# Optimization experiments

Measured on AMD Instinct MI355X. Metric: run time of the kernel, lower is better.

Reference implementation:

```python
import jax, jax.numpy as jnp
import numpy as np

B, S, E, H, FF = 4, 2048, 1024, 16, 4096
DK = E // H
EPS = 1e-5


def setup_inputs() -> dict:
    key = jax.random.key(0)
    ks = jax.random.split(key, 16)
    sc = 0.02
    return {
        "x": jax.random.normal(ks[0], (B, S, E), jnp.float32),
        "Wq": jax.random.normal(ks[1], (E, E), jnp.float32) * sc,
        "Wk": jax.random.normal(ks[2], (E, E), jnp.float32) * sc,
        "Wv": jax.random.normal(ks[3], (E, E), jnp.float32) * sc,
        "Wo": jax.random.normal(ks[4], (E, E), jnp.float32) * sc,
        "theta": jax.random.normal(ks[5], (DK,), jnp.float32),
        "Wcq": jax.random.normal(ks[6], (E, E), jnp.float32) * sc,
        "ln1_g": jnp.ones((E,), jnp.float32),
        "ln1_b": jnp.zeros((E,), jnp.float32),
        "W1": jax.random.normal(ks[7], (E, FF), jnp.float32) * sc,
        "b1": jnp.zeros((FF,), jnp.float32),
        "W2": jax.random.normal(ks[8], (FF, E), jnp.float32) * sc,
        "b2": jnp.zeros((E,), jnp.float32),
        "ln2_g": jnp.ones((E,), jnp.float32),
        "ln2_b": jnp.zeros((E,), jnp.float32),
    }


def _layernorm(x, g, b):
    mu = jnp.mean(x, axis=-1, keepdims=True)
    var = jnp.mean(jnp.square(x - mu), axis=-1, keepdims=True)
    return (x - mu) * jax.lax.rsqrt(var + EPS) * g + b


def reference(x, Wq, Wk, Wv, Wo, theta, Wcq, ln1_g, ln1_b, W1, b1, W2, b2, ln2_g, ln2_b):
    mix = 0.5
    # classical multi-head attention
    def heads(t):  # [B,S,E] -> [B,H,S,DK]
        return t.reshape(B, S, H, DK).transpose(0, 2, 1, 3)
    q = heads(x @ Wq)
    k = heads(x @ Wk)
    v = heads(x @ Wv)
    scores = jnp.einsum("bhqd,bhkd->bhqk", q, k) / jnp.sqrt(jnp.float32(DK))
    attn = jax.nn.softmax(scores, axis=-1)
    ctx = jnp.einsum("bhqk,bhkd->bhqd", attn, v)
    ctx = ctx.transpose(0, 2, 1, 3).reshape(B, S, E)
    classical = ctx @ Wo
    # quantum heads: RX(x)RX(theta)|0>, <Z> = cos(x + theta), same theta shared per head
    qh = jnp.cos(x.reshape(B, S, H, DK) + theta)  # broadcast over wires
    quantum = qh.reshape(B, S, E) @ Wcq
    attn_out = mix * classical + (1.0 - mix) * quantum
    x1 = _layernorm(x + attn_out, ln1_g, ln1_b)
    ffn = jax.nn.relu(x1 @ W1 + b1) @ W2 + b2
    return _layernorm(x1 + ffn, ln2_g, ln2_b)
```

## Files before the change

### kernel.cpp

```cpp
#include <hip/hip_runtime.h>
#include <hip/hip_bf16.h>

typedef __bf16 bf16_t;
typedef bf16_t bf16x8 __attribute__((ext_vector_type(8)));
typedef bf16_t bf16x4v __attribute__((ext_vector_type(4)));
typedef float f32x4 __attribute__((ext_vector_type(4)));

static constexpr int EE = 1024;
static constexpr int SS = 2048;
static constexpr int DK = 64;
static constexpr float QSCALE = 0.125f * 1.44269504f;

__device__ __forceinline__ void gload_lds16(const void* g, void* l) {
  __builtin_amdgcn_global_load_lds(
      (__attribute__((address_space(1))) void*)g,
      (__attribute__((address_space(3))) void*)l, 16, 0, 0);
}

__device__ __forceinline__ f32x4 mfma16(bf16x8 a, bf16x8 b, f32x4 c) {
  return __builtin_amdgcn_mfma_f32_16x16x32_bf16(a, b, c, 0, 0, 0);
}

__global__ void __launch_bounds__(256) prep_x_kernel(
    const float* __restrict__ x, const float* __restrict__ theta,
    bf16_t* __restrict__ xbf, bf16_t* __restrict__ A2)
{
  const long t = (long)blockIdx.x * 256 + threadIdx.x;
  const long e0 = t * 8;
  const int col = (int)(e0 & (EE - 1));
  const long row = e0 >> 10;
  const float4 v0 = *(const float4*)&x[e0];
  const float4 v1 = *(const float4*)&x[e0 + 4];
  float xs[8] = {v0.x, v0.y, v0.z, v0.w, v1.x, v1.y, v1.z, v1.w};
  const int d0 = col & (DK - 1);
  bf16x8 xb, qb;
#pragma unroll
  for (int j = 0; j < 8; ++j) {
    xb[j] = (bf16_t)xs[j];
    qb[j] = (bf16_t)__cosf(xs[j] + theta[d0 + j]);
  }
  *(bf16x8*)&xbf[e0] = xb;
  *(bf16x8*)&A2[row * 2048 + EE + col] = qb;
}

__global__ void __launch_bounds__(256) transpose_w_kernel(
    const float* __restrict__ src, bf16_t* __restrict__ dst,
    int N, long dstride, long dcol0)
{
  __shared__ float tile[32][33];
  const int tx = threadIdx.x, ty = threadIdx.y;
  const long n0 = (long)blockIdx.x * 32, k0 = (long)blockIdx.y * 32;
#pragma unroll
  for (int j = 0; j < 4; ++j)
    tile[ty + j * 8][tx] = src[(k0 + ty + j * 8) * N + n0 + tx];
  __syncthreads();
#pragma unroll
  for (int j = 0; j < 4; ++j)
    dst[(n0 + ty + j * 8) * dstride + dcol0 + k0 + tx] = (bf16_t)tile[tx][ty + j * 8];
}

template<int MODE>
__global__ void __launch_bounds__(256, 3) gemm_bt(
    const bf16_t* __restrict__ A, const bf16_t* __restrict__ Bt,
    void* __restrict__ C, int M, int N, int K,
    const float* __restrict__ aux1, const bf16_t* __restrict__ aux2)
{
  __shared__ bf16_t As[128 * 32];
  __shared__ bf16_t Bs[128 * 32];
  const int tid = threadIdx.x;
  const int lane = tid & 63, wid = tid >> 6;
  const int wr = wid >> 1, wc = wid & 1;
  const int lr = lane & 15, lk = lane >> 4;
  const int nwg = gridDim.x * gridDim.y;
  const int bid = blockIdx.y * gridDim.x + blockIdx.x;
  const int swz = (bid & 7) * (nwg >> 3) + (bid >> 3);
  const long m0 = (long)(swz / gridDim.x) * 128;
  const long n0 = (long)(swz % gridDim.x) * 128;
  f32x4 acc[4][4] = {};

  for (int k0 = 0; k0 < K; k0 += 32) {
#pragma unroll
    for (int j = 0; j < 2; ++j) {
      const int c = __builtin_amdgcn_readfirstlane(wid * 2 + j);
      const int e = c * 512 + lane * 8;
      const int row = e >> 5, colk = e & 31;
      gload_lds16(&A[(m0 + row) * K + k0 + colk], &As[c * 512]);
      gload_lds16(&Bt[(n0 + row) * K + k0 + colk], &Bs[c * 512]);
    }
    __syncthreads();
    bf16x8 af[4], bfr[4];
#pragma unroll
    for (int mb = 0; mb < 4; ++mb)
      af[mb] = *(const bf16x8*)&As[(wr * 64 + mb * 16 + lr) * 32 + lk * 8];
#pragma unroll
    for (int nb = 0; nb < 4; ++nb)
      bfr[nb] = *(const bf16x8*)&Bs[(wc * 64 + nb * 16 + lr) * 32 + lk * 8];
#pragma unroll
    for (int mb = 0; mb < 4; ++mb)
#pragma unroll
      for (int nb = 0; nb < 4; ++nb)
        acc[mb][nb] = mfma16(af[mb], bfr[nb], acc[mb][nb]);
    __syncthreads();
  }

#pragma unroll
  for (int mb = 0; mb < 4; ++mb)
#pragma unroll
    for (int nb = 0; nb < 4; ++nb)
#pragma unroll
      for (int i = 0; i < 4; ++i) {
        const long r = m0 + wr * 64 + mb * 16 + lk * 4 + i;
        const long cc = n0 + wc * 64 + nb * 16 + lr;
        float v = acc[mb][nb][i];
        if constexpr (MODE == 0) {
          if (cc < 1024) v *= QSCALE;
          ((bf16_t*)C)[r * N + cc] = (bf16_t)v;
        } else if constexpr (MODE == 1) {
          ((float*)C)[r * N + cc] = 0.5f * v + aux1[r * N + cc];
        } else if constexpr (MODE == 2) {
          ((bf16_t*)C)[r * N + cc] = (bf16_t)fmaxf(v + aux1[cc], 0.0f);
        } else {
          ((float*)C)[r * N + cc] = v + aux1[cc] + (float)aux2[r * N + cc];
        }
      }
}

__global__ void __launch_bounds__(256, 2) attn_kernel(
    const bf16_t* __restrict__ QKV, bf16_t* __restrict__ Ctx)
{
  __shared__ bf16_t Ks[2][64 * 72];
  __shared__ bf16_t Vt[2][64 * 72];
  const int tid = threadIdx.x;
  const int lane = tid & 63, w = tid >> 6;
  const int lr = lane & 15, lk = lane >> 4;
  const int bh = blockIdx.x, b = bh >> 4, h = bh & 15;
  const long rowbase = (long)b * SS;
  const int q0 = blockIdx.y * 128;
  const int qcol = h * 64, kcol = EE + h * 64, vcol = 2 * EE + h * 64;
  constexpr int NT = SS / 64;

  bf16x8 qf[2][2];
#pragma unroll
  for (int mb = 0; mb < 2; ++mb)
#pragma unroll
    for (int ks = 0; ks < 2; ++ks)
      qf[mb][ks] = *(const bf16x8*)&QKV[
          (rowbase + q0 + w * 32 + mb * 16 + lr) * 3072 + qcol + ks * 32 + lk * 8];

  const int sr = tid >> 3;
  const int g  = tid & 7;
  const int d0 = g * 8;

  bf16x8 kreg[2], vreg[2];
  auto load_kv = [&](int t) {
#pragma unroll
    for (int it = 0; it < 2; ++it) {
      const long r = rowbase + (long)t * 64 + sr + it * 32;
      kreg[it] = *(const bf16x8*)&QKV[r * 3072 + kcol + d0];
      vreg[it] = *(const bf16x8*)&QKV[r * 3072 + vcol + d0];
    }
  };
  auto write_kv = [&](int buf) {
#pragma unroll
    for (int it = 0; it < 2; ++it) {
      const int r = sr + it * 32;
      *(bf16x8*)&Ks[buf][r * 72 + d0] = kreg[it];
      const int sg = (r & 0x23) | ((r & 0x0C) << 1) | ((r & 0x10) >> 2);
      const int vbase = d0 * 72 + (((sg >> 3) + g) & 7) * 8 + (sg & 7);
#pragma unroll
      for (int jj = 0; jj < 8; ++jj)
        Vt[buf][vbase + jj * 72] = vreg[it][jj];
    }
  };

  f32x4 oacc[2][4] = {};
  float mrow[2] = {-3.0e38f, -3.0e38f};
  float lsum[2] = {0.0f, 0.0f};

  load_kv(0);
  write_kv(0);

  for (int t = 0; t < NT; ++t) {
    const int buf = t & 1;
    if (t + 1 < NT) load_kv(t + 1);
    __syncthreads();

    bf16x8 kf[4][2];
#pragma unroll
    for (int nb = 0; nb < 4; ++nb)
#pragma unroll
      for (int ks = 0; ks < 2; ++ks)
        kf[nb][ks] = *(const bf16x8*)&Ks[buf][(nb * 16 + lr) * 72 + ks * 32 + lk * 8];

    f32x4 sacc[2][4] = {};
    __builtin_amdgcn_s_setprio(1);
#pragma unroll
    for (int mb = 0; mb < 2; ++mb)
#pragma unroll
      for (int nb = 0; nb < 4; ++nb)
#pragma unroll
        for (int ks = 0; ks < 2; ++ks)
          sacc[mb][nb] = mfma16(kf[nb][ks], qf[mb][ks], sacc[mb][nb]);
    __builtin_amdgcn_s_setprio(0);

    bf16x8 vf[4][2];
#pragma unroll
    for (int nb = 0; nb < 4; ++nb)
#pragma unroll
      for (int ks = 0; ks < 2; ++ks) {
        const int dvr = nb * 16 + lr;
        vf[nb][ks] = *(const bf16x8*)&Vt[buf][dvr * 72 + (((ks * 4 + lk) + (dvr >> 3)) & 7) * 8];
      }

#pragma unroll
    for (int mb = 0; mb < 2; ++mb) {
      float t01, t23, tmax = -3.0e38f;
#pragma unroll
      for (int nb = 0; nb < 4; ++nb) {
        t01 = fmaxf(sacc[mb][nb][0], sacc[mb][nb][1]);
        t23 = fmaxf(sacc[mb][nb][2], sacc[mb][nb][3]);
        tmax = fmaxf(tmax, fmaxf(t01, t23));
      }
      if (!__all(tmax <= mrow[mb] + 8.0f)) {
        float rmax = tmax;
        rmax = fmaxf(rmax, __shfl_xor(rmax, 16));
        rmax = fmaxf(rmax, __shfl_xor(rmax, 32));
        const float mnew = fmaxf(mrow[mb], rmax);
        const float resc = exp2f(mrow[mb] - mnew);
        mrow[mb] = mnew;
        lsum[mb] *= resc;
        float ro[4];
#pragma unroll
        for (int i = 0; i < 4; ++i) ro[i] = __shfl(resc, lk * 4 + i);
#pragma unroll
        for (int nb = 0; nb < 4; ++nb)
#pragma unroll
          for (int i = 0; i < 4; ++i)
            oacc[mb][nb][i] *= ro[i];
      }
      const float m = mrow[mb];
      float psum = 0.0f;
      bf16x8 pf[2];
#pragma unroll
      for (int nb = 0; nb < 4; ++nb)
#pragma unroll
        for (int i = 0; i < 4; ++i) {
          const float pv = exp2f(sacc[mb][nb][i] - m);
          psum += pv;
          pf[nb >> 1][(nb & 1) * 4 + i] = (bf16_t)pv;
        }
      lsum[mb] += psum;
      __builtin_amdgcn_s_setprio(1);
#pragma unroll
      for (int nb = 0; nb < 4; ++nb)
#pragma unroll
        for (int ks = 0; ks < 2; ++ks)
          oacc[mb][nb] = mfma16(pf[ks], vf[nb][ks], oacc[mb][nb]);
      __builtin_amdgcn_s_setprio(0);
    }

    if (t + 1 < NT) write_kv((t + 1) & 1);
  }

#pragma unroll
  for (int mb = 0; mb < 2; ++mb) {
    float l = lsum[mb];
    l += __shfl_xor(l, 16);
    l += __shfl_xor(l, 32);
    float li[4];
#pragma unroll
    for (int i = 0; i < 4; ++i) li[i] = 1.0f / __shfl(l, lk * 4 + i);
#pragma unroll
    for (int nb = 0; nb < 4; ++nb)
#pragma unroll
      for (int i = 0; i < 4; ++i) {
        const long r = rowbase + q0 + w * 32 + mb * 16 + lk * 4 + i;
        Ctx[r * 2048 + h * 64 + nb * 16 + lr] = (bf16_t)(oacc[mb][nb][i] * li[i]);
      }
  }
}

__device__ __forceinline__ void ln_reduce(const float4& v, int tid,
                                          float& mu, float& rs) {
  float s = v.x + v.y + v.z + v.w;
  float ss = v.x * v.x + v.y * v.y + v.z * v.z + v.w * v.w;
#pragma unroll
  for (int off = 1; off < 64; off <<= 1) {
    s += __shfl_xor(s, off);
    ss += __shfl_xor(ss, off);
  }
  __shared__ float wsum[4], wsq[4];
  if ((tid & 63) == 0) { wsum[tid >> 6] = s; wsq[tid >> 6] = ss; }
  __syncthreads();
  s = wsum[0] + wsum[1] + wsum[2] + wsum[3];
  ss = wsq[0] + wsq[1] + wsq[2] + wsq[3];
  mu = s * (1.0f / EE);
  rs = rsqrtf(ss * (1.0f / EE) - mu * mu + 1e-5f);
}

__global__ void __launch_bounds__(256) ln_bf16_kernel(
    const float* __restrict__ pre, const float* __restrict__ g,
    const float* __restrict__ bt, bf16_t* __restrict__ out)
{
  const int r = blockIdx.x, tid = threadIdx.x;
  const long base = (long)r * EE + tid * 4;
  const float4 v = *(const float4*)&pre[base];
  float mu, rs;
  ln_reduce(v, tid, mu, rs);
  const float4 gv = *(const float4*)&g[tid * 4];
  const float4 bv = *(const float4*)&bt[tid * 4];
  bf16x4v o;
  o[0] = (bf16_t)((v.x - mu) * rs * gv.x + bv.x);
  o[1] = (bf16_t)((v.y - mu) * rs * gv.y + bv.y);
  o[2] = (bf16_t)((v.z - mu) * rs * gv.z + bv.z);
  o[3] = (bf16_t)((v.w - mu) * rs * gv.w + bv.w);
  *(bf16x4v*)&out[base] = o;
}

__global__ void __launch_bounds__(256) ln_f32_kernel(
    const float* __restrict__ pre, const float* __restrict__ g,
    const float* __restrict__ bt, float* __restrict__ out)
{
  const int r = blockIdx.x, tid = threadIdx.x;
  const long base = (long)r * EE + tid * 4;
  const float4 v = *(const float4*)&pre[base];
  float mu, rs;
  ln_reduce(v, tid, mu, rs);
  const float4 gv = *(const float4*)&g[tid * 4];
  const float4 bv = *(const float4*)&bt[tid * 4];
  float4 o;
  o.x = (v.x - mu) * rs * gv.x + bv.x;
  o.y = (v.y - mu) * rs * gv.y + bv.y;
  o.z = (v.z - mu) * rs * gv.z + bv.z;
  o.w = (v.w - mu) * rs * gv.w + bv.w;
  *(float4*)&out[base] = o;
}

extern "C" void kernel_launch(void* const* d_in, const int* in_sizes, int n_in,
                              void* d_out, int out_size, void* d_ws, size_t ws_size,
                              hipStream_t stream)
{
  (void)in_sizes; (void)n_in; (void)out_size; (void)ws_size;
  const float* x     = (const float*)d_in[0];
  const float* Wq    = (const float*)d_in[1];
  const float* Wk    = (const float*)d_in[2];
  const float* Wv    = (const float*)d_in[3];
  const float* Wo    = (const float*)d_in[4];
  const float* theta = (const float*)d_in[5];
  const float* Wcq   = (const float*)d_in[6];
  const float* ln1g  = (const float*)d_in[7];
  const float* ln1b  = (const float*)d_in[8];
  const float* W1    = (const float*)d_in[9];
  const float* b1    = (const float*)d_in[10];
  const float* W2    = (const float*)d_in[11];
  const float* b2    = (const float*)d_in[12];
  const float* ln2g  = (const float*)d_in[13];
  const float* ln2b  = (const float*)d_in[14];

  char* ws = (char*)d_ws;
  const size_t MB = 1ull << 20;
  bf16_t* xbf    = (bf16_t*)(ws + 0);
  bf16_t* QKV    = (bf16_t*)(ws + 16 * MB);
  float*  preLN1 = (float*)(ws + 16 * MB);
  bf16_t* A2     = (bf16_t*)(ws + 64 * MB);
  float*  preLN2 = (float*)(ws + 64 * MB);
  bf16_t* H1     = (bf16_t*)(ws + 96 * MB);
  bf16_t* BtQKV  = (bf16_t*)(ws + 160 * MB);
  bf16_t* Bt2    = (bf16_t*)(ws + 166 * MB);
  bf16_t* BtW1   = (bf16_t*)(ws + 170 * MB);
  bf16_t* BtW2   = (bf16_t*)(ws + 178 * MB);

  dim3 tb(32, 8);
  prep_x_kernel<<<4096, 256, 0, stream>>>(x, theta, xbf, A2);
  transpose_w_kernel<<<dim3(32, 32), tb, 0, stream>>>(Wq,  BtQKV,              1024, 1024, 0);
  transpose_w_kernel<<<dim3(32, 32), tb, 0, stream>>>(Wk,  BtQKV + 1024*1024,  1024, 1024, 0);
  transpose_w_kernel<<<dim3(32, 32), tb, 0, stream>>>(Wv,  BtQKV + 2048*1024,  1024, 1024, 0);
  transpose_w_kernel<<<dim3(32, 32), tb, 0, stream>>>(Wo,  Bt2,  1024, 2048, 0);
  transpose_w_kernel<<<dim3(32, 32), tb, 0, stream>>>(Wcq, Bt2,  1024, 2048, 1024);
  transpose_w_kernel<<<dim3(128, 32), tb, 0, stream>>>(W1, BtW1, 4096, 1024, 0);
  transpose_w_kernel<<<dim3(32, 128), tb, 0, stream>>>(W2, BtW2, 1024, 4096, 0);

  gemm_bt<0><<<dim3(24, 64), 256, 0, stream>>>(xbf, BtQKV, QKV, 8192, 3072, 1024, nullptr, nullptr);
  attn_kernel<<<dim3(64, 16), 256, 0, stream>>>(QKV, A2);
  gemm_bt<1><<<dim3(8, 64), 256, 0, stream>>>(A2, Bt2, preLN1, 8192, 1024, 2048, x, nullptr);
  ln_bf16_kernel<<<8192, 256, 0, stream>>>(preLN1, ln1g, ln1b, xbf);
  gemm_bt<2><<<dim3(32, 64), 256, 0, stream>>>(xbf, BtW1, H1, 8192, 4096, 1024, b1, nullptr);
  gemm_bt<3><<<dim3(8, 64), 256, 0, stream>>>(H1, BtW2, preLN2, 8192, 1024, 4096, b2, xbf);
  ln_f32_kernel<<<8192, 256, 0, stream>>>(preLN2, ln2g, ln2b, (float*)d_out);
}
```

Baseline: 500.2 us.

## Add 256x256-tile 4-stage pipelined GEMM for QKV and FFN1 projections

Adds a new GEMM kernel with 256x256 output tiles, 512 threads, a 4-stage LDS ring buffer filled by direct global-to-LDS loads, XOR-swizzled LDS layout, and split MFMA phases that interleave prefetch with compute under raised wave priority. The QKV projection and the first FFN GEMM switch to this kernel. The larger tiles and deeper prefetch are meant to raise data reuse and hide global-load latency. The cost is much higher LDS use (128 KB per block) and more registers, which may cap occupancy, and the larger tiles yield fewer workgroups per launch.

```diff
diff --git a/kernel.cpp b/kernel.cpp
--- a/kernel.cpp
+++ b/kernel.cpp
@@ -57,6 +57,114 @@
 #pragma unroll
   for (int j = 0; j < 4; ++j)
     dst[(n0 + ty + j * 8) * dstride + dcol0 + k0 + tx] = (bf16_t)tile[tx][ty + j * 8];
+}
+
+template<int MODE>
+__global__ void __launch_bounds__(512, 2) gemm256(
+    const bf16_t* __restrict__ A, const bf16_t* __restrict__ Bt,
+    void* __restrict__ C, int M, int N, int K,
+    const float* __restrict__ aux1)
+{
+  __shared__ bf16_t As[4][256 * 32];
+  __shared__ bf16_t Bs[4][256 * 32];
+  const int tid = threadIdx.x;
+  const int lane = tid & 63, wid = tid >> 6;
+  const int wr = wid >> 2, wc = wid & 3;
+  const int lr = lane & 15, lk = lane >> 4;
+  const int gx = gridDim.x;
+  const int nwg = gx * gridDim.y;
+  const int bid = blockIdx.y * gx + blockIdx.x;
+  const int swz = (bid & 7) * (nwg >> 3) + (bid >> 3);
+  const long m0 = (long)(swz / gx) * 256;
+  const long n0 = (long)(swz % gx) * 256;
+
+  const int r0 = (wid * 2 + 0) * 16 + (lane >> 2);
+  const int r1 = (wid * 2 + 1) * 16 + (lane >> 2);
+  const int sl = lane & 3;
+  const bf16_t* sA0 = &A [(m0 + r0) * K + 8 * (sl ^ (r0 & 3))];
+  const bf16_t* sA1 = &A [(m0 + r1) * K + 8 * (sl ^ (r1 & 3))];
+  const bf16_t* sB0 = &Bt[(n0 + r0) * K + 8 * (sl ^ (r0 & 3))];
+  const bf16_t* sB1 = &Bt[(n0 + r1) * K + 8 * (sl ^ (r1 & 3))];
+  const int lo = wid * 1024;
+
+  f32x4 acc[8][4] = {};
+  const int NKT = K / 32;
+
+  auto stA = [&](int t) {
+    const int s = t & 3;
+    gload_lds16(sA0 + (long)t * 32, &As[s][lo]);
+    gload_lds16(sA1 + (long)t * 32, &As[s][lo + 512]);
+  };
+  auto stB = [&](int t) {
+    const int s = t & 3;
+    gload_lds16(sB0 + (long)t * 32, &Bs[s][lo]);
+    gload_lds16(sB1 + (long)t * 32, &Bs[s][lo + 512]);
+  };
+
+  stA(0); stB(0); stA(1); stB(1); stA(2); stB(2);
+  asm volatile("s_waitcnt vmcnt(8)" ::: "memory");
+  __builtin_amdgcn_s_barrier();
+
+  for (int t = 0; t < NKT; ++t) {
+    const int s = t & 3;
+    bf16x8 bfr[4], af[4];
+#pragma unroll
+    for (int nb = 0; nb < 4; ++nb) {
+      const int rw = wc * 64 + nb * 16 + lr;
+      bfr[nb] = *(const bf16x8*)&Bs[s][rw * 32 + (lk ^ (rw & 3)) * 8];
+    }
+#pragma unroll
+    for (int mb = 0; mb < 4; ++mb) {
+      const int rw = wr * 128 + mb * 16 + lr;
+      af[mb] = *(const bf16x8*)&As[s][rw * 32 + (lk ^ (rw & 3)) * 8];
+    }
+    if (t + 3 < NKT) stA(t + 3);
+    asm volatile("s_waitcnt lgkmcnt(0)" ::: "memory");
+    __builtin_amdgcn_sched_barrier(0);
+    __builtin_amdgcn_s_setprio(1);
+#pragma unroll
+    for (int mb = 0; mb < 4; ++mb)
+#pragma unroll
+      for (int nb = 0; nb < 4; ++nb)
+        acc[mb][nb] = mfma16(af[mb], bfr[nb], acc[mb][nb]);
+    __builtin_amdgcn_s_setprio(0);
+#pragma unroll
+    for (int mb = 0; mb < 4; ++mb) {
+      const int rw = wr * 128 + 64 + mb * 16 + lr;
+      af[mb] = *(const bf16x8*)&As[s][rw * 32 + (lk ^ (rw & 3)) * 8];
+    }
+    if (t + 3 < NKT) stB(t + 3);
+    asm volatile("s_waitcnt lgkmcnt(0)" ::: "memory");
+    __builtin_amdgcn_sched_barrier(0);
+    __builtin_amdgcn_s_setprio(1);
+#pragma unroll
+    for (int mb = 0; mb < 4; ++mb)
+#pragma unroll
+      for (int nb = 0; nb < 4; ++nb)
+        acc[mb + 4][nb] = mfma16(af[mb], bfr[nb], acc[mb + 4][nb]);
+    __builtin_amdgcn_s_setprio(0);
+    if (t + 3 < NKT)        { asm volatile("s_waitcnt vmcnt(8)" ::: "memory"); }
+    else if (t + 3 == NKT)  { asm volatile("s_waitcnt vmcnt(4)" ::: "memory"); }
+    else if (t + 2 == NKT)  { asm volatile("s_waitcnt vmcnt(0)" ::: "memory"); }
+    __builtin_amdgcn_s_barrier();
+  }
+
+#pragma unroll
+  for (int mb = 0; mb < 8; ++mb)
+#pragma unroll
+    for (int nb = 0; nb < 4; ++nb)
+#pragma unroll
+      for (int i = 0; i < 4; ++i) {
+        const long r = m0 + wr * 128 + mb * 16 + lk * 4 + i;
+        const long cc = n0 + wc * 64 + nb * 16 + lr;
+        float v = acc[mb][nb][i];
+        if constexpr (MODE == 0) {
+          if (cc < 1024) v *= QSCALE;
+          ((bf16_t*)C)[r * N + cc] = (bf16_t)v;
+        } else {
+          ((bf16_t*)C)[r * N + cc] = (bf16_t)fmaxf(v + aux1[cc], 0.0f);
+        }
+      }
 }
 
 template<int MODE>
@@ -112,13 +220,8 @@
         const long r = m0 + wr * 64 + mb * 16 + lk * 4 + i;
         const long cc = n0 + wc * 64 + nb * 16 + lr;
         float v = acc[mb][nb][i];
-        if constexpr (MODE == 0) {
-          if (cc < 1024) v *= QSCALE;
-          ((bf16_t*)C)[r * N + cc] = (bf16_t)v;
-        } else if constexpr (MODE == 1) {
+        if constexpr (MODE == 1) {
           ((float*)C)[r * N + cc] = 0.5f * v + aux1[r * N + cc];
-        } else if constexpr (MODE == 2) {
-          ((bf16_t*)C)[r * N + cc] = (bf16_t)fmaxf(v + aux1[cc], 0.0f);
         } else {
           ((float*)C)[r * N + cc] = v + aux1[cc] + (float)aux2[r * N + cc];
         }
@@ -380,11 +483,11 @@
   transpose_w_kernel<<<dim3(128, 32), tb, 0, stream>>>(W1, BtW1, 4096, 1024, 0);
   transpose_w_kernel<<<dim3(32, 128), tb, 0, stream>>>(W2, BtW2, 1024, 4096, 0);
 
-  gemm_bt<0><<<dim3(24, 64), 256, 0, stream>>>(xbf, BtQKV, QKV, 8192, 3072, 1024, nullptr, nullptr);
+  gemm256<0><<<dim3(12, 32), 512, 0, stream>>>(xbf, BtQKV, QKV, 8192, 3072, 1024, nullptr);
   attn_kernel<<<dim3(64, 16), 256, 0, stream>>>(QKV, A2);
   gemm_bt<1><<<dim3(8, 64), 256, 0, stream>>>(A2, Bt2, preLN1, 8192, 1024, 2048, x, nullptr);
   ln_bf16_kernel<<<8192, 256, 0, stream>>>(preLN1, ln1g, ln1b, xbf);
-  gemm_bt<2><<<dim3(32, 64), 256, 0, stream>>>(xbf, BtW1, H1, 8192, 4096, 1024, b1, nullptr);
+  gemm256<2><<<dim3(16, 32), 512, 0, stream>>>(xbf, BtW1, H1, 8192, 4096, 1024, b1);
   gemm_bt<3><<<dim3(8, 64), 256, 0, stream>>>(H1, BtW2, preLN2, 8192, 1024, 4096, b2, xbf);
   ln_f32_kernel<<<8192, 256, 0, stream>>>(preLN2, ln2g, ln2b, (float*)d_out);
 }
```

Result: no change. 499.7 us (-0.1%).
